# Kernel optimization log

Measured on AMD Instinct MI355X. Metric: run time of the kernel, lower is better.

The kernel has to match this reference:

```python
import jax, jax.numpy as jnp
import numpy as np
import math

HIDDEN = 2048
NUM_HEADS = 16
HEAD_SIZE = HIDDEN // NUM_HEADS
BATCH = 2
SEQ = 2048


def setup_inputs() -> dict:
    key = jax.random.key(0)
    k_x, k_wq, k_bq, k_wo, k_bo = jax.random.split(key, 5)
    scale_in = 1.0 / math.sqrt(HIDDEN)
    return {
        "x": jax.random.normal(k_x, (BATCH, SEQ, HIDDEN), dtype=jnp.float32),
        # torch Linear stored as W[out,in]; we keep the jax-friendly transpose [in,out]
        "Wqkv": jax.random.normal(k_wq, (HIDDEN, 3 * HIDDEN), dtype=jnp.float32) * scale_in,
        "bqkv": jax.random.normal(k_bq, (3 * HIDDEN,), dtype=jnp.float32) * 0.01,
        "Wo": jax.random.normal(k_wo, (HIDDEN, HIDDEN), dtype=jnp.float32) * scale_in,
        "bo": jax.random.normal(k_bo, (HIDDEN,), dtype=jnp.float32) * 0.01,
    }


def reference(x, Wqkv, bqkv, Wo, bo):
    b, s, _ = x.shape
    # fused QKV projection; channel layout is (three, num_heads, head_size)
    kqv = x @ Wqkv + bqkv                      # [b, s, 3*hidden]
    kqv = kqv.reshape(b, s, 3, NUM_HEADS, HEAD_SIZE)
    q = kqv[:, :, 0]                           # [b, s, n, h]
    k = kqv[:, :, 1]
    v = kqv[:, :, 2]
    # scores[b, n, s_key, t_query] = K_s . Q_t, scaled
    scores = jnp.einsum('bsnh,btnh->bnst', k, q) / math.sqrt(HEAD_SIZE)
    # faithful to original: keep upper triangle (key <= query), masked entries are exactly -10000
    ones = jnp.ones_like(scores)
    scores = jnp.triu(scores) + (-10000.0) * jnp.tril(ones, k=-1)
    attn = jax.nn.softmax(scores, axis=2)      # softmax over key dim
    out = jnp.einsum('bnkq,bknh->bqnh', attn, v)  # [b, s, n, h]
    out = out.reshape(b, s, NUM_HEADS * HEAD_SIZE)
    return out @ Wo + bo
```

## Files before the change

kernel.cpp:

```cpp
#include <hip/hip_runtime.h>
#include <hip/hip_bf16.h>

typedef __hip_bfloat16 bf16;
typedef __attribute__((ext_vector_type(8))) short short8;
typedef __attribute__((ext_vector_type(8))) unsigned short ushort8;
typedef __attribute__((ext_vector_type(4))) float floatx4;

#define BATCH 2
#define S_LEN 2048
#define NHEAD 16
#define HD 128
#define HIDDEN 2048
#define QSCALE 0.12754435f
#define FOFF 12.0f

static __device__ __forceinline__ unsigned short f2bf(float f) {
    union { float f; unsigned int u; } c; c.f = f;
    unsigned int u = c.u;
    unsigned int rounded = u + 0x7FFF + ((u >> 16) & 1);
    return (unsigned short)(rounded >> 16);
}

__global__ __launch_bounds__(256) void cast_f32_bf16(const float* __restrict__ src,
                                                     bf16* __restrict__ dst) {
    int i = (blockIdx.x * 256 + threadIdx.x) * 8;
    float4 a = *(const float4*)&src[i];
    float4 b = *(const float4*)&src[i + 4];
    ushort8 o;
    o[0] = f2bf(a.x); o[1] = f2bf(a.y); o[2] = f2bf(a.z); o[3] = f2bf(a.w);
    o[4] = f2bf(b.x); o[5] = f2bf(b.y); o[6] = f2bf(b.z); o[7] = f2bf(b.w);
    *(ushort8*)&dst[i] = o;
}

__global__ __launch_bounds__(256) void cast_transpose(const float* __restrict__ src,
                                                      bf16* __restrict__ dst,
                                                      int R, int C) {
    __shared__ unsigned short t[32][33];
    int tx = threadIdx.x & 31, ty = threadIdx.x >> 5;
    int c0 = blockIdx.x * 32, r0 = blockIdx.y * 32;
#pragma unroll
    for (int i = 0; i < 4; i++) {
        int r = r0 + ty + i * 8;
        t[ty + i * 8][tx] = f2bf(src[(size_t)r * C + c0 + tx]);
    }
    __syncthreads();
#pragma unroll
    for (int i = 0; i < 4; i++) {
        int cc = c0 + ty + i * 8;
        ((unsigned short*)dst)[(size_t)cc * R + r0 + tx] = t[tx][ty + i * 8];
    }
}

__global__ __launch_bounds__(256) void gemm_bt(const bf16* __restrict__ A,
                                               const bf16* __restrict__ Bt,
                                               const float* __restrict__ bias,
                                               bf16* __restrict__ Qb,
                                               bf16* __restrict__ Kb,
                                               bf16* __restrict__ Vt,
                                               int K, int noff) {
    __shared__ __align__(16) bf16 As[128 * 32];
    __shared__ __align__(16) bf16 Bs[128 * 32];

    int tid = threadIdx.x;
    int wave = tid >> 6, lane = tid & 63;
    int quad = lane >> 4, lr = lane & 15;
    int wm = wave >> 1, wn = wave & 1;
    int m0 = blockIdx.y * 128, n0 = blockIdx.x * 128 + noff;

    const floatx4 fzero = {0.f, 0.f, 0.f, 0.f};
    floatx4 acc[4][4];
#pragma unroll
    for (int i = 0; i < 4; i++)
#pragma unroll
        for (int j = 0; j < 4; j++) acc[i][j] = fzero;

    int rsub = lane >> 2;
    int csub = (lane & 3) * 8;
    const bf16* gA0 = A + (size_t)(m0 + wave * 32 + rsub) * K + csub;
    const bf16* gA1 = gA0 + (size_t)16 * K;
    const bf16* gB0 = Bt + (size_t)(n0 + wave * 32 + rsub) * K + csub;
    const bf16* gB1 = gB0 + (size_t)16 * K;
    bf16* lA0 = As + wave * 1024;
    bf16* lA1 = As + wave * 1024 + 512;
    bf16* lB0 = Bs + wave * 1024;
    bf16* lB1 = Bs + wave * 1024 + 512;

    for (int kt = 0; kt < K; kt += 32) {
        __builtin_amdgcn_global_load_lds(
            (const __attribute__((address_space(1))) void*)(gA0 + kt),
            (__attribute__((address_space(3))) void*)lA0, 16, 0, 0);
        __builtin_amdgcn_global_load_lds(
            (const __attribute__((address_space(1))) void*)(gA1 + kt),
            (__attribute__((address_space(3))) void*)lA1, 16, 0, 0);
        __builtin_amdgcn_global_load_lds(
            (const __attribute__((address_space(1))) void*)(gB0 + kt),
            (__attribute__((address_space(3))) void*)lB0, 16, 0, 0);
        __builtin_amdgcn_global_load_lds(
            (const __attribute__((address_space(1))) void*)(gB1 + kt),
            (__attribute__((address_space(3))) void*)lB1, 16, 0, 0);
        __syncthreads();

        short8 aF[4], bF[4];
#pragma unroll
        for (int i = 0; i < 4; i++)
            aF[i] = *(const short8*)(As + (wm * 64 + i * 16 + lr) * 32 + quad * 8);
#pragma unroll
        for (int j = 0; j < 4; j++)
            bF[j] = *(const short8*)(Bs + (wn * 64 + j * 16 + lr) * 32 + quad * 8);
#pragma unroll
        for (int i = 0; i < 4; i++)
#pragma unroll
            for (int j = 0; j < 4; j++)
                acc[i][j] = __builtin_amdgcn_mfma_f32_16x16x32_bf16(aF[i], bF[j], acc[i][j], 0, 0, 0);
        __syncthreads();
    }

#pragma unroll
    for (int i = 0; i < 4; i++) {
#pragma unroll
        for (int j = 0; j < 4; j++) {
            int gcn = n0 + wn * 64 + j * 16 + lr;
            float bv = bias[gcn];
#pragma unroll
            for (int reg = 0; reg < 4; reg++) {
                int gm = m0 + wm * 64 + i * 16 + quad * 4 + reg;
                float v = acc[i][j][reg] + bv;
                int t = gcn >> 11, hh = (gcn >> 7) & 15, d = gcn & 127;
                int bb = gm >> 11, s = gm & 2047;
                size_t hb = (size_t)(bb * NHEAD + hh);
                if (t == 0) {
                    Qb[(hb * S_LEN + s) * HD + d] = __float2bfloat16(v * QSCALE);
                } else if (t == 1) {
                    Kb[(hb * S_LEN + s) * HD + d] = __float2bfloat16(v);
                } else {
                    Vt[(hb * HD + d) * S_LEN + s] = __float2bfloat16(v);
                }
            }
        }
    }
}

__global__ __launch_bounds__(256) void gemm_out(const bf16* __restrict__ A,
                                                const bf16* __restrict__ Bt,
                                                const float* __restrict__ bias,
                                                float* __restrict__ C,
                                                int N, int K) {
    __shared__ __align__(16) bf16 As[128 * 32];
    __shared__ __align__(16) bf16 Bs[128 * 32];

    int tid = threadIdx.x;
    int wave = tid >> 6, lane = tid & 63;
    int quad = lane >> 4, lr = lane & 15;
    int wm = wave >> 1, wn = wave & 1;
    int m0 = blockIdx.y * 128, n0 = blockIdx.x * 128;

    const floatx4 fzero = {0.f, 0.f, 0.f, 0.f};
    floatx4 acc[4][4];
#pragma unroll
    for (int i = 0; i < 4; i++)
#pragma unroll
        for (int j = 0; j < 4; j++) acc[i][j] = fzero;

    int rsub = lane >> 2;
    int csub = (lane & 3) * 8;
    const bf16* gA0 = A + (size_t)(m0 + wave * 32 + rsub) * K + csub;
    const bf16* gA1 = gA0 + (size_t)16 * K;
    const bf16* gB0 = Bt + (size_t)(n0 + wave * 32 + rsub) * K + csub;
    const bf16* gB1 = gB0 + (size_t)16 * K;
    bf16* lA0 = As + wave * 1024;
    bf16* lA1 = As + wave * 1024 + 512;
    bf16* lB0 = Bs + wave * 1024;
    bf16* lB1 = Bs + wave * 1024 + 512;

    for (int kt = 0; kt < K; kt += 32) {
        __builtin_amdgcn_global_load_lds(
            (const __attribute__((address_space(1))) void*)(gA0 + kt),
            (__attribute__((address_space(3))) void*)lA0, 16, 0, 0);
        __builtin_amdgcn_global_load_lds(
            (const __attribute__((address_space(1))) void*)(gA1 + kt),
            (__attribute__((address_space(3))) void*)lA1, 16, 0, 0);
        __builtin_amdgcn_global_load_lds(
            (const __attribute__((address_space(1))) void*)(gB0 + kt),
            (__attribute__((address_space(3))) void*)lB0, 16, 0, 0);
        __builtin_amdgcn_global_load_lds(
            (const __attribute__((address_space(1))) void*)(gB1 + kt),
            (__attribute__((address_space(3))) void*)lB1, 16, 0, 0);
        __syncthreads();

        short8 aF[4], bF[4];
#pragma unroll
        for (int i = 0; i < 4; i++)
            aF[i] = *(const short8*)(As + (wm * 64 + i * 16 + lr) * 32 + quad * 8);
#pragma unroll
        for (int j = 0; j < 4; j++)
            bF[j] = *(const short8*)(Bs + (wn * 64 + j * 16 + lr) * 32 + quad * 8);
#pragma unroll
        for (int i = 0; i < 4; i++)
#pragma unroll
            for (int j = 0; j < 4; j++)
                acc[i][j] = __builtin_amdgcn_mfma_f32_16x16x32_bf16(aF[i], bF[j], acc[i][j], 0, 0, 0);
        __syncthreads();
    }

#pragma unroll
    for (int i = 0; i < 4; i++) {
#pragma unroll
        for (int j = 0; j < 4; j++) {
            int gcn = n0 + wn * 64 + j * 16 + lr;
            float bv = bias[gcn];
#pragma unroll
            for (int reg = 0; reg < 4; reg++) {
                int gm = m0 + wm * 64 + i * 16 + quad * 4 + reg;
                C[(size_t)gm * N + gcn] = acc[i][j][reg] + bv;
            }
        }
    }
}

#define PSTR 72
__global__ __launch_bounds__(256, 2) void attn_kernel(const bf16* __restrict__ Qb,
                                                      const bf16* __restrict__ Kb,
                                                      const bf16* __restrict__ Vt,
                                                      bf16* __restrict__ Obuf) {
    __shared__ __align__(16) bf16 Ks[64 * 128];
    __shared__ __align__(16) bf16 Vs[128 * 64];
    __shared__ __align__(16) bf16 Ps[4][16 * PSTR];

    int tid = threadIdx.x;
    int wave = tid >> 6, lane = tid & 63;
    int quad = lane >> 4, lr = lane & 15;
    int srow = lane >> 4;
    int head = blockIdx.x, p = blockIdx.y, b = blockIdx.z;
    size_t hb = (size_t)(b * NHEAD + head);
    const bf16* Qbase = Qb + hb * S_LEN * HD;
    const bf16* Kbase = Kb + hb * S_LEN * HD;
    const bf16* Vbase = Vt + hb * (size_t)HD * S_LEN;

    const floatx4 fzero = {0.f, 0.f, 0.f, 0.f};
    const float MASKV = -30000.f;
    short8 ones;
#pragma unroll
    for (int i = 0; i < 8; i++) ones[i] = (short)0x3F80;

    for (int sub = 0; sub < 2; sub++) {
        int qt = sub ? (31 - p) : p;
        int q0 = qt * 64;
        int niter = qt + 1;

        short8 qF[4];
#pragma unroll
        for (int kc = 0; kc < 4; kc++)
            qF[kc] = *(const short8*)&Qbase[(size_t)(q0 + wave * 16 + lr) * HD + kc * 32 + quad * 8];

        floatx4 Oacc[8];
        floatx4 lacc = fzero;
#pragma unroll
        for (int dn = 0; dn < 8; dn++) Oacc[dn] = fzero;

        ushort8 kpre[4], vpre[4];
#pragma unroll
        for (int i = 0; i < 4; i++) {
            int rl = wave * 16 + i * 4 + srow;
            int gc = lr ^ (rl & 15);
            kpre[i] = *(const ushort8*)&Kbase[(size_t)rl * HD + gc * 8];
            int vr = wave * 32 + i * 8 + (lane >> 3);
            int gvc = (lane & 7) ^ (vr & 7);
            vpre[i] = *(const ushort8*)&Vbase[(size_t)vr * S_LEN + gvc * 8];
        }

        for (int kt = 0; kt < niter; kt++) {
            __syncthreads();
#pragma unroll
            for (int i = 0; i < 4; i++) {
                *(ushort8*)&Ks[(wave * 16 + i * 4) * 128 + lane * 8] = kpre[i];
                *(ushort8*)&Vs[(wave * 32 + i * 8) * 64 + lane * 8] = vpre[i];
            }
            __syncthreads();
            if (kt + 1 < niter) {
                int ns0 = (kt + 1) * 64;
#pragma unroll
                for (int i = 0; i < 4; i++) {
                    int rl = wave * 16 + i * 4 + srow;
                    int gc = lr ^ (rl & 15);
                    kpre[i] = *(const ushort8*)&Kbase[(size_t)(ns0 + rl) * HD + gc * 8];
                    int vr = wave * 32 + i * 8 + (lane >> 3);
                    int gvc = (lane & 7) ^ (vr & 7);
                    vpre[i] = *(const ushort8*)&Vbase[(size_t)vr * S_LEN + ns0 + gvc * 8];
                }
            }

            floatx4 sc[4];
#pragma unroll
            for (int nt = 0; nt < 4; nt++) sc[nt] = fzero;
#pragma unroll
            for (int kc = 0; kc < 4; kc++)
#pragma unroll
                for (int nt = 0; nt < 4; nt++) {
                    short8 kf = *(const short8*)&Ks[(nt * 16 + lr) * 128 + (((kc * 4 + quad) ^ lr) & 15) * 8];
                    sc[nt] = __builtin_amdgcn_mfma_f32_16x16x32_bf16(qF[kc], kf, sc[nt], 0, 0, 0);
                }
            if (kt == niter - 1) {
#pragma unroll
                for (int nt = 0; nt < 4; nt++)
#pragma unroll
                    for (int reg = 0; reg < 4; reg++) {
                        int qg = wave * 16 + quad * 4 + reg;
                        int kg = nt * 16 + lr;
                        if (kg > qg) sc[nt][reg] = MASKV;
                    }
            }
#pragma unroll
            for (int nt = 0; nt < 4; nt++)
#pragma unroll
                for (int reg = 0; reg < 4; reg++) {
                    float pv = __builtin_amdgcn_exp2f(sc[nt][reg] - FOFF);
                    Ps[wave][(quad * 4 + reg) * PSTR + nt * 16 + lr] = __float2bfloat16(pv);
                }
#pragma unroll
            for (int st = 0; st < 2; st++) {
                short8 aP = *(const short8*)&Ps[wave][lr * PSTR + st * 32 + quad * 8];
                lacc = __builtin_amdgcn_mfma_f32_16x16x32_bf16(aP, ones, lacc, 0, 0, 0);
#pragma unroll
                for (int dn = 0; dn < 8; dn++) {
                    short8 vf = *(const short8*)&Vs[(dn * 16 + lr) * 64 + (((st * 4 + quad) ^ (lr & 7)) & 7) * 8];
                    Oacc[dn] = __builtin_amdgcn_mfma_f32_16x16x32_bf16(aP, vf, Oacc[dn], 0, 0, 0);
                }
            }
        }

#pragma unroll
        for (int reg = 0; reg < 4; reg++) {
            float inv = 1.0f / lacc[reg];
            int qg = q0 + wave * 16 + quad * 4 + reg;
#pragma unroll
            for (int dn = 0; dn < 8; dn++) {
                int d = dn * 16 + lr;
                Obuf[((size_t)(b * S_LEN + qg)) * HIDDEN + head * HD + d] =
                    __float2bfloat16(Oacc[dn][reg] * inv);
            }
        }
    }
}

extern "C" void kernel_launch(void* const* d_in, const int* in_sizes, int n_in,
                              void* d_out, int out_size, void* d_ws, size_t ws_size,
                              hipStream_t stream) {
    (void)in_sizes; (void)n_in; (void)out_size; (void)ws_size;
    const float* x    = (const float*)d_in[0];
    const float* Wqkv = (const float*)d_in[1];
    const float* bqkv = (const float*)d_in[2];
    const float* Wo   = (const float*)d_in[3];
    const float* bo   = (const float*)d_in[4];
    float* out = (float*)d_out;

    bf16* ws = (bf16*)d_ws;
    bf16* Xb    = ws;
    bf16* Obuf  = ws;
    bf16* WqkvT = ws + (size_t)8388608;
    bf16* WoT   = WqkvT;
    bf16* Qb    = WqkvT + (size_t)12582912;
    bf16* Kb    = Qb + (size_t)8388608;
    bf16* Vt    = Kb + (size_t)8388608;

    cast_f32_bf16<<<4096, 256, 0, stream>>>(x, Xb);
    cast_transpose<<<dim3(192, 64), 256, 0, stream>>>(Wqkv, WqkvT, 2048, 6144);
    gemm_bt<<<dim3(24, 32), 256, 0, stream>>>(Xb, WqkvT, bqkv, Qb, Kb, Vt, 2048, 0);
    gemm_bt<<<dim3(24, 32), 256, 0, stream>>>(Xb, WqkvT, bqkv, Qb, Kb, Vt, 2048, 3072);
    cast_transpose<<<dim3(64, 64), 256, 0, stream>>>(Wo, WoT, 2048, 2048);
    attn_kernel<<<dim3(16, 16, 2), 256, 0, stream>>>(Qb, Kb, Vt, Obuf);
    gemm_out<<<dim3(16, 32), 256, 0, stream>>>(Obuf, WoT, bo, out, 2048, 2048);
}
```

Measured before the change: 408.5 us.

## Replace 128x128 GEMMs with double-buffered 256x256 swizzled-LDS GEMM kernel

Both projection GEMMs move from a 128x128, 256-thread, single-buffered kernel to a templated 256x256-tile, 512-thread kernel. The new kernel uses BK=64, double-buffered LDS fed by direct global-to-LDS loads, an XOR-swizzled LDS layout, a phased MFMA schedule with setprio, and a block-index swizzle for cache locality. The QKV GEMM now runs as one launch instead of two. The aim is more data reuse per tile and overlap of loads with MFMA. The cost is higher register and LDS pressure (128KB LDS per block) and fewer blocks (128 for the output GEMM), which may underfill the GPU's compute units.

```diff
diff --git a/kernel.cpp b/kernel.cpp
--- a/kernel.cpp
+++ b/kernel.cpp
@@ -51,167 +51,159 @@
     }
 }
 
-__global__ __launch_bounds__(256) void gemm_bt(const bf16* __restrict__ A,
-                                               const bf16* __restrict__ Bt,
-                                               const float* __restrict__ bias,
-                                               bf16* __restrict__ Qb,
-                                               bf16* __restrict__ Kb,
-                                               bf16* __restrict__ Vt,
-                                               int K, int noff) {
-    __shared__ __align__(16) bf16 As[128 * 32];
-    __shared__ __align__(16) bf16 Bs[128 * 32];
+#define GK 2048
+#define NT 32
+
+#define STG(pG, lG, s, h)                                                       \
+    do {                                                                        \
+        __builtin_amdgcn_global_load_lds(                                       \
+            (const __attribute__((address_space(1))) void*)(pG + (size_t)((h) * 128) * GK + (s) * 64), \
+            (__attribute__((address_space(3))) void*)(lG + ((s) & 1) * 32768 + (h) * 16384 + ldst),    \
+            16, 0, 0);                                                          \
+        __builtin_amdgcn_global_load_lds(                                       \
+            (const __attribute__((address_space(1))) void*)(pG + (size_t)((h) * 128 + 64) * GK + (s) * 64), \
+            (__attribute__((address_space(3))) void*)(lG + ((s) & 1) * 32768 + (h) * 16384 + 8192 + ldst), \
+            16, 0, 0);                                                          \
+    } while (0)
+
+#define LDA(i, ks) (*(const short8*)(Ab + ((((wm * 128 + (i) * 16 + lr) << 7) + (ks) * 64 + quad * 16) ^ axor)))
+#define LDB(j, ks) (*(const short8*)(Bb + ((((wn * 64 + (j) * 16 + lr) << 7) + (ks) * 64 + quad * 16) ^ axor)))
+
+#define PHASE_MFMA(IOFF, BF, JOFF)                                              \
+    __builtin_amdgcn_s_setprio(1);                                              \
+    _Pragma("unroll")                                                           \
+    for (int ks = 0; ks < 2; ks++)                                              \
+        _Pragma("unroll")                                                       \
+        for (int i = 0; i < 4; i++)                                             \
+            _Pragma("unroll")                                                   \
+            for (int j = 0; j < 2; j++)                                         \
+                acc[(IOFF) + i][(JOFF) + j] = __builtin_amdgcn_mfma_f32_16x16x32_bf16( \
+                    aF[i][ks], BF[j][ks], acc[(IOFF) + i][(JOFF) + j], 0, 0, 0); \
+    __builtin_amdgcn_s_setprio(0);
+
+#define BAR __builtin_amdgcn_s_barrier()
+#define LGKM0 asm volatile("s_waitcnt lgkmcnt(0)" ::: "memory")
+
+template <int EPI>
+__global__ __launch_bounds__(512, 2) void gemm256(const bf16* __restrict__ A,
+                                                  const bf16* __restrict__ Bt,
+                                                  const float* __restrict__ bias,
+                                                  bf16* __restrict__ Qb,
+                                                  bf16* __restrict__ Kb,
+                                                  bf16* __restrict__ Vt,
+                                                  float* __restrict__ Cout,
+                                                  int ntN) {
+    __shared__ __align__(16) bf16 Asm[2][256 * 64];
+    __shared__ __align__(16) bf16 Bsm[2][256 * 64];
 
     int tid = threadIdx.x;
     int wave = tid >> 6, lane = tid & 63;
     int quad = lane >> 4, lr = lane & 15;
-    int wm = wave >> 1, wn = wave & 1;
-    int m0 = blockIdx.y * 128, n0 = blockIdx.x * 128 + noff;
+    int wm = wave >> 2, wn = wave & 3;
+    int axor = (lr & 7) << 4;
+
+    int nwg = gridDim.x;
+    int cpx = nwg >> 3;
+    int bid = blockIdx.x;
+    int swz = (bid & 7) * cpx + (bid >> 3);
+    int mt = swz / ntN, nt = swz - mt * ntN;
+    int m0 = mt * 256, n0 = nt * 256;
+
+    int srow = wave * 8 + (lane >> 3);
+    int scol = ((lane & 7) ^ ((lane >> 3) & 7)) * 8;
+    const bf16* pA = A + (size_t)(m0 + srow) * GK + scol;
+    const bf16* pB = Bt + (size_t)(n0 + srow) * GK + scol;
+    char* lA = (char*)&Asm[0][0];
+    char* lB = (char*)&Bsm[0][0];
+    int ldst = wave * 1024;
 
     const floatx4 fzero = {0.f, 0.f, 0.f, 0.f};
-    floatx4 acc[4][4];
-#pragma unroll
-    for (int i = 0; i < 4; i++)
+    floatx4 acc[8][4];
+#pragma unroll
+    for (int i = 0; i < 8; i++)
 #pragma unroll
         for (int j = 0; j < 4; j++) acc[i][j] = fzero;
 
-    int rsub = lane >> 2;
-    int csub = (lane & 3) * 8;
-    const bf16* gA0 = A + (size_t)(m0 + wave * 32 + rsub) * K + csub;
-    const bf16* gA1 = gA0 + (size_t)16 * K;
-    const bf16* gB0 = Bt + (size_t)(n0 + wave * 32 + rsub) * K + csub;
-    const bf16* gB1 = gB0 + (size_t)16 * K;
-    bf16* lA0 = As + wave * 1024;
-    bf16* lA1 = As + wave * 1024 + 512;
-    bf16* lB0 = Bs + wave * 1024;
-    bf16* lB1 = Bs + wave * 1024 + 512;
-
-    for (int kt = 0; kt < K; kt += 32) {
-        __builtin_amdgcn_global_load_lds(
-            (const __attribute__((address_space(1))) void*)(gA0 + kt),
-            (__attribute__((address_space(3))) void*)lA0, 16, 0, 0);
-        __builtin_amdgcn_global_load_lds(
-            (const __attribute__((address_space(1))) void*)(gA1 + kt),
-            (__attribute__((address_space(3))) void*)lA1, 16, 0, 0);
-        __builtin_amdgcn_global_load_lds(
-            (const __attribute__((address_space(1))) void*)(gB0 + kt),
-            (__attribute__((address_space(3))) void*)lB0, 16, 0, 0);
-        __builtin_amdgcn_global_load_lds(
-            (const __attribute__((address_space(1))) void*)(gB1 + kt),
-            (__attribute__((address_space(3))) void*)lB1, 16, 0, 0);
-        __syncthreads();
-
-        short8 aF[4], bF[4];
-#pragma unroll
-        for (int i = 0; i < 4; i++)
-            aF[i] = *(const short8*)(As + (wm * 64 + i * 16 + lr) * 32 + quad * 8);
-#pragma unroll
-        for (int j = 0; j < 4; j++)
-            bF[j] = *(const short8*)(Bs + (wn * 64 + j * 16 + lr) * 32 + quad * 8);
-#pragma unroll
-        for (int i = 0; i < 4; i++)
-#pragma unroll
-            for (int j = 0; j < 4; j++)
-                acc[i][j] = __builtin_amdgcn_mfma_f32_16x16x32_bf16(aF[i], bF[j], acc[i][j], 0, 0, 0);
-        __syncthreads();
-    }
-
-#pragma unroll
-    for (int i = 0; i < 4; i++) {
-#pragma unroll
-        for (int j = 0; j < 4; j++) {
-            int gcn = n0 + wn * 64 + j * 16 + lr;
-            float bv = bias[gcn];
-#pragma unroll
-            for (int reg = 0; reg < 4; reg++) {
-                int gm = m0 + wm * 64 + i * 16 + quad * 4 + reg;
-                float v = acc[i][j][reg] + bv;
-                int t = gcn >> 11, hh = (gcn >> 7) & 15, d = gcn & 127;
-                int bb = gm >> 11, s = gm & 2047;
-                size_t hb = (size_t)(bb * NHEAD + hh);
-                if (t == 0) {
-                    Qb[(hb * S_LEN + s) * HD + d] = __float2bfloat16(v * QSCALE);
-                } else if (t == 1) {
-                    Kb[(hb * S_LEN + s) * HD + d] = __float2bfloat16(v);
-                } else {
-                    Vt[(hb * HD + d) * S_LEN + s] = __float2bfloat16(v);
-                }
-            }
-        }
-    }
-}
-
-__global__ __launch_bounds__(256) void gemm_out(const bf16* __restrict__ A,
-                                                const bf16* __restrict__ Bt,
-                                                const float* __restrict__ bias,
-                                                float* __restrict__ C,
-                                                int N, int K) {
-    __shared__ __align__(16) bf16 As[128 * 32];
-    __shared__ __align__(16) bf16 Bs[128 * 32];
-
-    int tid = threadIdx.x;
-    int wave = tid >> 6, lane = tid & 63;
-    int quad = lane >> 4, lr = lane & 15;
-    int wm = wave >> 1, wn = wave & 1;
-    int m0 = blockIdx.y * 128, n0 = blockIdx.x * 128;
-
-    const floatx4 fzero = {0.f, 0.f, 0.f, 0.f};
-    floatx4 acc[4][4];
-#pragma unroll
-    for (int i = 0; i < 4; i++)
-#pragma unroll
-        for (int j = 0; j < 4; j++) acc[i][j] = fzero;
-
-    int rsub = lane >> 2;
-    int csub = (lane & 3) * 8;
-    const bf16* gA0 = A + (size_t)(m0 + wave * 32 + rsub) * K + csub;
-    const bf16* gA1 = gA0 + (size_t)16 * K;
-    const bf16* gB0 = Bt + (size_t)(n0 + wave * 32 + rsub) * K + csub;
-    const bf16* gB1 = gB0 + (size_t)16 * K;
-    bf16* lA0 = As + wave * 1024;
-    bf16* lA1 = As + wave * 1024 + 512;
-    bf16* lB0 = Bs + wave * 1024;
-    bf16* lB1 = Bs + wave * 1024 + 512;
-
-    for (int kt = 0; kt < K; kt += 32) {
-        __builtin_amdgcn_global_load_lds(
-            (const __attribute__((address_space(1))) void*)(gA0 + kt),
-            (__attribute__((address_space(3))) void*)lA0, 16, 0, 0);
-        __builtin_amdgcn_global_load_lds(
-            (const __attribute__((address_space(1))) void*)(gA1 + kt),
-            (__attribute__((address_space(3))) void*)lA1, 16, 0, 0);
-        __builtin_amdgcn_global_load_lds(
-            (const __attribute__((address_space(1))) void*)(gB0 + kt),
-            (__attribute__((address_space(3))) void*)lB0, 16, 0, 0);
-        __builtin_amdgcn_global_load_lds(
-            (const __attribute__((address_space(1))) void*)(gB1 + kt),
-            (__attribute__((address_space(3))) void*)lB1, 16, 0, 0);
-        __syncthreads();
-
-        short8 aF[4], bF[4];
-#pragma unroll
-        for (int i = 0; i < 4; i++)
-            aF[i] = *(const short8*)(As + (wm * 64 + i * 16 + lr) * 32 + quad * 8);
-#pragma unroll
-        for (int j = 0; j < 4; j++)
-            bF[j] = *(const short8*)(Bs + (wn * 64 + j * 16 + lr) * 32 + quad * 8);
-#pragma unroll
-        for (int i = 0; i < 4; i++)
-#pragma unroll
-            for (int j = 0; j < 4; j++)
-                acc[i][j] = __builtin_amdgcn_mfma_f32_16x16x32_bf16(aF[i], bF[j], acc[i][j], 0, 0, 0);
-        __syncthreads();
-    }
-
-#pragma unroll
-    for (int i = 0; i < 4; i++) {
-#pragma unroll
-        for (int j = 0; j < 4; j++) {
-            int gcn = n0 + wn * 64 + j * 16 + lr;
-            float bv = bias[gcn];
-#pragma unroll
-            for (int reg = 0; reg < 4; reg++) {
-                int gm = m0 + wm * 64 + i * 16 + quad * 4 + reg;
-                C[(size_t)gm * N + gcn] = acc[i][j][reg] + bv;
+    short8 aF[4][2], b0F[2][2], b1F[2][2];
+
+    STG(pB, lB, 0, 0); STG(pB, lB, 0, 1); STG(pA, lA, 0, 0); STG(pA, lA, 0, 1);
+    STG(pB, lB, 1, 0); STG(pB, lB, 1, 1); STG(pA, lA, 1, 0); STG(pA, lA, 1, 1);
+    asm volatile("s_waitcnt vmcnt(8)" ::: "memory");
+    BAR;
+
+    for (int t = 0; t < NT; ++t) {
+        const char* Ab = lA + (t & 1) * 32768;
+        const char* Bb = lB + (t & 1) * 32768;
+
+#pragma unroll
+        for (int i = 0; i < 4; i++) { aF[i][0] = LDA(i, 0); aF[i][1] = LDA(i, 1); }
+#pragma unroll
+        for (int j = 0; j < 2; j++) { b0F[j][0] = LDB(j, 0); b0F[j][1] = LDB(j, 1); }
+        BAR; LGKM0;
+        PHASE_MFMA(0, b0F, 0)
+        BAR;
+
+#pragma unroll
+        for (int j = 0; j < 2; j++) { b1F[j][0] = LDB(j + 2, 0); b1F[j][1] = LDB(j + 2, 1); }
+        BAR; LGKM0;
+        PHASE_MFMA(0, b1F, 2)
+        BAR;
+
+#pragma unroll
+        for (int i = 0; i < 4; i++) { aF[i][0] = LDA(i + 4, 0); aF[i][1] = LDA(i + 4, 1); }
+        if (t + 2 < NT) { STG(pB, lB, t + 2, 0); STG(pB, lB, t + 2, 1); }
+        BAR; LGKM0;
+        PHASE_MFMA(4, b1F, 2)
+        BAR;
+
+        if (t + 2 < NT) {
+            STG(pA, lA, t + 2, 0); STG(pA, lA, t + 2, 1);
+            asm volatile("s_waitcnt vmcnt(8)" ::: "memory");
+        } else {
+            asm volatile("s_waitcnt vmcnt(0)" ::: "memory");
+        }
+        BAR;
+        PHASE_MFMA(4, b0F, 0)
+        BAR;
+    }
+
+    if (EPI == 0) {
+#pragma unroll
+        for (int i = 0; i < 8; i++) {
+#pragma unroll
+            for (int j = 0; j < 4; j++) {
+                int gcn = n0 + wn * 64 + j * 16 + lr;
+                float bv = bias[gcn];
+                int tsel = gcn >> 11, hh = (gcn >> 7) & 15, d = gcn & 127;
+#pragma unroll
+                for (int reg = 0; reg < 4; reg++) {
+                    int gm = m0 + wm * 128 + i * 16 + quad * 4 + reg;
+                    float v = acc[i][j][reg] + bv;
+                    int bb = gm >> 11, s = gm & 2047;
+                    size_t hb = (size_t)(bb * NHEAD + hh);
+                    if (tsel == 0) {
+                        Qb[(hb * S_LEN + s) * HD + d] = __float2bfloat16(v * QSCALE);
+                    } else if (tsel == 1) {
+                        Kb[(hb * S_LEN + s) * HD + d] = __float2bfloat16(v);
+                    } else {
+                        Vt[(hb * HD + d) * S_LEN + s] = __float2bfloat16(v);
+                    }
+                }
+            }
+        }
+    } else {
+        int N = ntN << 8;
+#pragma unroll
+        for (int i = 0; i < 8; i++) {
+#pragma unroll
+            for (int j = 0; j < 4; j++) {
+                int gcn = n0 + wn * 64 + j * 16 + lr;
+                float bv = bias[gcn];
+#pragma unroll
+                for (int reg = 0; reg < 4; reg++) {
+                    int gm = m0 + wm * 128 + i * 16 + quad * 4 + reg;
+                    Cout[(size_t)gm * N + gcn] = acc[i][j][reg] + bv;
+                }
             }
         }
     }
@@ -364,9 +356,8 @@
 
     cast_f32_bf16<<<4096, 256, 0, stream>>>(x, Xb);
     cast_transpose<<<dim3(192, 64), 256, 0, stream>>>(Wqkv, WqkvT, 2048, 6144);
-    gemm_bt<<<dim3(24, 32), 256, 0, stream>>>(Xb, WqkvT, bqkv, Qb, Kb, Vt, 2048, 0);
-    gemm_bt<<<dim3(24, 32), 256, 0, stream>>>(Xb, WqkvT, bqkv, Qb, Kb, Vt, 2048, 3072);
+    gemm256<0><<<dim3(384), dim3(512), 0, stream>>>(Xb, WqkvT, bqkv, Qb, Kb, Vt, nullptr, 24);
     cast_transpose<<<dim3(64, 64), 256, 0, stream>>>(Wo, WoT, 2048, 2048);
     attn_kernel<<<dim3(16, 16, 2), 256, 0, stream>>>(Qb, Kb, Vt, Obuf);
-    gemm_out<<<dim3(16, 32), 256, 0, stream>>>(Obuf, WoT, bo, out, 2048, 2048);
-}
+    gemm256<1><<<dim3(128), dim3(512), 0, stream>>>(Obuf, WoT, bo, nullptr, nullptr, nullptr, out, 8);
+}
```

New measurement: 420.7 us. +3.0%, slower.
